# Optimization experiments

Hardware: AMD Instinct MI355X
Metric: run time of the kernel (lower is better)

The kernel has to match this reference:

```python
import jax, jax.numpy as jnp
import numpy as np

B, T, D, H, DK, DV, C, M = 8, 512, 1024, 8, 128, 128, 512, 512
TAU = float(DK) ** 0.5

def _ln(x, g, b, eps=1e-6):
    mu = x.mean(-1, keepdims=True)
    var = ((x - mu) ** 2).mean(-1, keepdims=True)
    return (x - mu) * jax.lax.rsqrt(var + eps) * g + b

def _hln(x, eps=1e-6):
    mu = x.mean(-1, keepdims=True)
    var = ((x - mu) ** 2).mean(-1, keepdims=True)
    return (x - mu) * jax.lax.rsqrt(var + eps)

def setup_inputs() -> dict:
    key = jax.random.key(0)
    ks = jax.random.split(key, 14)
    s = lambda k, shape, fan: jax.random.normal(k, shape, jnp.float32) * (fan ** -0.5)
    return {
        "x": jax.random.normal(ks[0], (B, T, D), jnp.float32),
        "doc_ids": jax.random.randint(ks[1], (B, T), 0, 4),
        "loss_mask": jnp.ones((B, T), jnp.float32),
        "xl_k_hat": jax.random.normal(ks[2], (B, H, M, DK), jnp.float32),
        "xl_v": jax.random.normal(ks[3], (B, H, M, DV), jnp.float32),
        "agg_upper": jax.random.normal(ks[4], (B, H, C, DV), jnp.float32),
        "agg_lower": jax.random.uniform(ks[5], (B, H, C), jnp.float32) * 8.0,
        "w_ln_g": jnp.ones((D,), jnp.float32),
        "w_ln_b": jnp.zeros((D,), jnp.float32),
        "w_q": s(ks[6], (D, H * DK), D),
        "w_k": s(ks[7], (D, H * DK), D),
        "w_v": s(ks[8], (D, H * DV), D),
        "w_g": s(ks[9], (D, H * DV), D),
        "w_res": s(ks[10], (H * DV, D), H * DV),
        "x_u": jax.random.normal(ks[11], (H, DK), jnp.float32) * 0.02,
        "codebook": jax.random.normal(ks[12], (H, C, DK), jnp.float32),
    }

def reference(x, doc_ids, loss_mask, xl_k_hat, xl_v, agg_upper, agg_lower,
              w_ln_g, w_ln_b, w_q, w_k, w_v, w_g, w_res, x_u, codebook):
    # ---- compute_k_q_v_g ----
    xt = _ln(x, w_ln_g, w_ln_b)                                  # [B,T,D]
    q = _hln((xt @ w_q).reshape(B, T, H, DK).transpose(0, 2, 1, 3))  # [B,H,T,DK]
    k = _hln((xt @ w_k).reshape(B, T, H, DK).transpose(0, 2, 1, 3))  # [B,H,T,DK]
    v = (xt @ w_v).reshape(B, T, H, DV).transpose(0, 2, 1, 3)        # [B,H,T,DV]
    g = jax.nn.silu(xt @ w_g)                                        # [B,T,H*DV]

    # ---- vector quantize keys (LearnableVQ) ----
    # dist[b,h,t,c] = ||k - codebook||^2 ; argmin -> shortcodes z
    kc = jnp.einsum('bhtd,hcd->bhtc', k, codebook)
    dist = (k ** 2).sum(-1)[..., None] - 2.0 * kc + (codebook ** 2).sum(-1)[None, :, None, :]
    z = jnp.argmin(dist, axis=-1)                                 # [B,H,T] shortcodes
    k_hat = codebook[jnp.arange(H)[None, :, None], z]             # [B,H,T,DK]
    k_hat_st = k + jax.lax.stop_gradient(k_hat - k)               # straight-through
    mask = loss_mask[:, None, :]                                  # [B,1,T]
    denom_m = mask.sum() * H + 1e-6
    l_commit = (((k - jax.lax.stop_gradient(k_hat)) ** 2).sum(-1) * mask).sum() / denom_m
    l_codebook = (((jax.lax.stop_gradient(k) - k_hat) ** 2).sum(-1) * mask).sum() / denom_m

    # ---- attention over xlcache ++ present, plus aggregated codeword cache ----
    recent_k = jnp.concatenate([xl_k_hat, k_hat_st], axis=2)      # [B,H,M+T,DK]
    recent_v = jnp.concatenate([xl_v, v], axis=2)                 # [B,H,M+T,DV]
    qb = q + x_u[None, :, None, :]
    s_rec = jnp.einsum('bhtd,bhsd->bhts', qb, recent_k) / TAU     # [B,H,T,M+T]
    s_agg = jnp.einsum('bhtd,hcd->bhtc', qb, codebook) / TAU      # [B,H,T,C]

    i = jnp.arange(T)[:, None]
    j = jnp.arange(M + T)[None, :]
    allow = ((j - M) <= i).astype(s_rec.dtype)                    # causal over recent window
    NEG = jnp.asarray(-1e30, s_rec.dtype)
    s_rec_m = jnp.where(allow > 0, s_rec, NEG)

    m = jnp.maximum(s_rec_m.max(-1), s_agg.max(-1))               # [B,H,T]
    a_rec = jnp.exp(s_rec_m - m[..., None]) * allow               # [B,H,T,M+T]
    a_agg = jnp.exp(s_agg - m[..., None])                         # [B,H,T,C]
    den = a_rec.sum(-1) + jnp.einsum('bhtc,bhc->bht', a_agg, agg_lower)
    num = (jnp.einsum('bhts,bhsd->bhtd', a_rec, recent_v)
           + jnp.einsum('bhtc,bhcd->bhtd', a_agg, agg_upper))
    wv = num / den[..., None]                                     # [B,H,T,DV]

    o = wv.transpose(0, 2, 1, 3).reshape(B, T, H * DV) * g        # gated
    res = o @ w_res                                               # [B,T,D]
    return res, l_commit, l_codebook
```

## Files before the change

### kernel.cpp

```cpp
#include <hip/hip_runtime.h>
#include <math.h>

namespace {

constexpr int nB = 8, nT = 512, nD = 1024, nH = 8, nDK = 128, nDV = 128, nC = 512, nM = 512;
constexpr int NROW = nB * nT;
constexpr float RTAU = 0.08838834764831845f;

typedef __attribute__((ext_vector_type(8))) short short8;
typedef __attribute__((ext_vector_type(4))) float f32x4;

__device__ __forceinline__ ushort f2bf(float f) {
  union { float f; uint u; } x; x.f = f;
  uint r = x.u + 0x7fff + ((x.u >> 16) & 1);
  return (ushort)(r >> 16);
}
__device__ __forceinline__ uint pk2(float a, float b) {
  return (uint)f2bf(a) | ((uint)f2bf(b) << 16);
}
__device__ __forceinline__ float bf2f(ushort u) {
  return __uint_as_float(((uint)u) << 16);
}
__device__ __forceinline__ void gload16(const void* g, void* l) {
  __builtin_amdgcn_global_load_lds((const __attribute__((address_space(1))) void*)g,
                                   (__attribute__((address_space(3))) void*)l, 16, 0, 0);
}

constexpr int PREP_LN = 4096;
constexpr int PREP_CAST = PREP_LN + 12288;
constexpr int PREP_WT = PREP_CAST + 1280;
constexpr int PREP_CB = PREP_WT + 2048;

__global__ __launch_bounds__(256) void prep_kernel(
    const float* __restrict__ x, const float* __restrict__ gw, const float* __restrict__ bw,
    ushort* __restrict__ xt_bf,
    const float* __restrict__ xlk, ushort* __restrict__ xlk_bf,
    const float* __restrict__ xlv, ushort* __restrict__ xlv_bf,
    const float* __restrict__ aggU, ushort* __restrict__ aggU_bf,
    const float* __restrict__ wq, const float* __restrict__ wk, const float* __restrict__ wv,
    const float* __restrict__ wg, const float* __restrict__ wres,
    ushort* __restrict__ wqkvg_t, ushort* __restrict__ wres_t,
    const float* __restrict__ cb, float* __restrict__ cbn, ushort* __restrict__ cb_bf) {
  __shared__ float tile[64][65];
  __shared__ float smc[4];
  const int bid = blockIdx.x;
  const int tid = threadIdx.x;

  if (bid < PREP_LN) {
    size_t row = bid;
    float4 v = ((const float4*)(x + row * nD))[tid];
    {
      int lane = tid & 63, w = tid >> 6;
      float s = v.x + v.y + v.z + v.w;
#pragma unroll
      for (int off = 32; off; off >>= 1) s += __shfl_down(s, off);
      if (lane == 0) smc[w] = s;
    }
    __syncthreads();
    float mu = (smc[0] + smc[1] + smc[2] + smc[3]) * (1.f / nD);
    __syncthreads();
    float4 d = make_float4(v.x - mu, v.y - mu, v.z - mu, v.w - mu);
    {
      int lane = tid & 63, w = tid >> 6;
      float s = d.x * d.x + d.y * d.y + d.z * d.z + d.w * d.w;
#pragma unroll
      for (int off = 32; off; off >>= 1) s += __shfl_down(s, off);
      if (lane == 0) smc[w] = s;
    }
    __syncthreads();
    float var = (smc[0] + smc[1] + smc[2] + smc[3]) * (1.f / nD);
    float rs = rsqrtf(var + 1e-6f);
    float4 gg = ((const float4*)gw)[tid];
    float4 bb = ((const float4*)bw)[tid];
    uint2 pb;
    pb.x = pk2(d.x * rs * gg.x + bb.x, d.y * rs * gg.y + bb.y);
    pb.y = pk2(d.z * rs * gg.z + bb.z, d.w * rs * gg.w + bb.w);
    ((uint2*)(xt_bf + row * nD))[tid] = pb;
  } else if (bid < PREP_CAST) {
    const int i = bid - PREP_LN;
    const int which = i >> 12, blk = i & 4095;
    const float* src = which == 0 ? xlk : (which == 1 ? xlv : aggU);
    ushort* dst = which == 0 ? xlk_bf : (which == 1 ? xlv_bf : aggU_bf);
    size_t idx = (size_t)blk * 256 + tid;
    float4 v = ((const float4*)src)[idx];
    uint2 p;
    p.x = pk2(v.x, v.y);
    p.y = pk2(v.z, v.w);
    ((uint2*)dst)[idx] = p;
  } else if (bid < PREP_WT) {
    const int i = bid - PREP_CAST;
    const int z = i >> 8, rem = i & 255;
    const int kz = (rem >> 4) * 64, nz = (rem & 15) * 64;
    const float* W;
    ushort* D;
    if (z == 0)      { W = wq;   D = wqkvg_t; }
    else if (z == 1) { W = wk;   D = wqkvg_t + (size_t)1024 * 1024; }
    else if (z == 2) { W = wv;   D = wqkvg_t + (size_t)2048 * 1024; }
    else if (z == 3) { W = wg;   D = wqkvg_t + (size_t)3072 * 1024; }
    else             { W = wres; D = wres_t; }
    const int c = tid & 63, r4 = tid >> 6;
#pragma unroll
    for (int k = 0; k < 16; ++k) {
      int r = k * 4 + r4;
      tile[r][c] = W[(size_t)(kz + r) * 1024 + nz + c];
    }
    __syncthreads();
#pragma unroll
    for (int k = 0; k < 16; ++k) {
      int n = k * 4 + r4;
      D[(size_t)(nz + n) * 1024 + kz + c] = f2bf(tile[c][n]);
    }
  } else {
    const int i = bid - PREP_WT;
    const int grp = tid >> 7, t128 = tid & 127;
    const int hc = i * 2 + grp;
    float v = cb[(size_t)hc * 128 + t128];
    cb_bf[(size_t)hc * 128 + t128] = f2bf(v);
    float s = v * v;
#pragma unroll
    for (int off = 32; off; off >>= 1) s += __shfl_down(s, off);
    if ((t128 & 63) == 0) smc[grp * 2 + (t128 >> 6)] = s;
    __syncthreads();
    if (t128 == 0) cbn[hc] = smc[grp * 2] + smc[grp * 2 + 1];
  }
}

template <int MODE>
__global__ __launch_bounds__(256) void gemm_bf16_kernel(const ushort* __restrict__ A,
                                                        const ushort* __restrict__ Bt,
                                                        float* __restrict__ C0,
                                                        ushort* __restrict__ C1,
                                                        ushort* __restrict__ C2,
                                                        ushort* __restrict__ C3) {
  __shared__ __align__(16) ushort As[128 * 32];
  __shared__ __align__(16) ushort Bs[128 * 32];
  const int tid = threadIdx.x;
  const int w = tid >> 6, l = tid & 63;
  const int lr = l & 15, lg = l >> 4;
  const int wr = w >> 1, wc = w & 1;
  const int n0 = blockIdx.x * 128;
  const int m0 = blockIdx.y * 128;
  constexpr int K = 1024;

  f32x4 acc[4][4];
#pragma unroll
  for (int i = 0; i < 4; ++i)
#pragma unroll
    for (int j = 0; j < 4; ++j) acc[i][j] = (f32x4){0.f, 0.f, 0.f, 0.f};

  const int e0 = w * 512 + l * 8;
  const int r0 = e0 >> 5, c0 = e0 & 31;
  const int e1 = 2048 + e0;
  const int r1 = e1 >> 5, c1 = e1 & 31;
  const ushort* a0p = A + (size_t)(m0 + r0) * K + c0;
  const ushort* a1p = A + (size_t)(m0 + r1) * K + c1;
  const ushort* b0p = Bt + (size_t)(n0 + r0) * K + c0;
  const ushort* b1p = Bt + (size_t)(n0 + r1) * K + c1;
  ushort* lA0 = &As[w * 512];
  ushort* lA1 = &As[2048 + w * 512];
  ushort* lB0 = &Bs[w * 512];
  ushort* lB1 = &Bs[2048 + w * 512];

  for (int k0 = 0; k0 < K; k0 += 32) {
    __syncthreads();
    gload16(a0p + k0, lA0);
    gload16(a1p + k0, lA1);
    gload16(b0p + k0, lB0);
    gload16(b1p + k0, lB1);
    __syncthreads();
    short8 af[4], bfr[4];
#pragma unroll
    for (int i = 0; i < 4; ++i) af[i] = *(const short8*)&As[(wr * 64 + i * 16 + lr) * 32 + lg * 8];
#pragma unroll
    for (int j = 0; j < 4; ++j) bfr[j] = *(const short8*)&Bs[(wc * 64 + j * 16 + lr) * 32 + lg * 8];
    __builtin_amdgcn_s_setprio(1);
#pragma unroll
    for (int i = 0; i < 4; ++i)
#pragma unroll
      for (int j = 0; j < 4; ++j)
        acc[i][j] = __builtin_amdgcn_mfma_f32_16x16x32_bf16(af[i], bfr[j], acc[i][j], 0, 0, 0);
    __builtin_amdgcn_s_setprio(0);
  }

  const int seg = n0 >> 10;
  const int nbase = n0 & 1023;
#pragma unroll
  for (int i = 0; i < 4; ++i)
#pragma unroll
    for (int j = 0; j < 4; ++j)
#pragma unroll
      for (int r2 = 0; r2 < 4; ++r2) {
        const int row = m0 + wr * 64 + i * 16 + lg * 4 + r2;
        const int col = wc * 64 + j * 16 + lr;
        float v = acc[i][j][r2];
        if (MODE == 0) {
          C0[(size_t)row * 1024 + n0 + col] = v;
        } else {
          const int nloc = nbase + col;
          if (seg == 0)      C1[(size_t)row * 1024 + nloc] = f2bf(v);
          else if (seg == 1) C0[(size_t)row * 1024 + nloc] = v;
          else if (seg == 2) C2[(size_t)row * 1024 + nloc] = f2bf(v);
          else {
            float s = v / (1.f + __expf(-v));
            C3[(size_t)row * 1024 + nloc] = f2bf(s);
          }
        }
      }
}

__global__ __launch_bounds__(256) void hln_both_kernel(ushort* __restrict__ qbuf,
                                                       const float* __restrict__ xu,
                                                       float* __restrict__ kbuf,
                                                       ushort* __restrict__ kbf,
                                                       float* __restrict__ knorm2) {
  int lane = threadIdx.x & 63;
  size_t row = (size_t)blockIdx.x * 4 + (threadIdx.x >> 6);
  if (blockIdx.y == 0) {
    ushort* p = qbuf + row * 128;
    uint u = *(uint*)(p + lane * 2);
    float vx = bf2f((ushort)(u & 0xffff)), vy = bf2f((ushort)(u >> 16));
    float s = vx + vy;
#pragma unroll
    for (int off = 32; off; off >>= 1) s += __shfl_down(s, off);
    float mu = __shfl(s, 0) * (1.f / 128.f);
    float dx = vx - mu, dy = vy - mu;
    float q = dx * dx + dy * dy;
#pragma unroll
    for (int off = 32; off; off >>= 1) q += __shfl_down(q, off);
    float rs = rsqrtf(__shfl(q, 0) * (1.f / 128.f) + 1e-6f);
    int h = (int)(row & 7);
    float ox = dx * rs + xu[h * 128 + lane * 2];
    float oy = dy * rs + xu[h * 128 + lane * 2 + 1];
    *(uint*)(p + lane * 2) = pk2(ox, oy);
  } else {
    float* p = kbuf + row * 128;
    float2 v = *(float2*)(p + lane * 2);
    float s = v.x + v.y;
#pragma unroll
    for (int off = 32; off; off >>= 1) s += __shfl_down(s, off);
    float mu = __shfl(s, 0) * (1.f / 128.f);
    float dx = v.x - mu, dy = v.y - mu;
    float q = dx * dx + dy * dy;
#pragma unroll
    for (int off = 32; off; off >>= 1) q += __shfl_down(q, off);
    float qf = __shfl(q, 0);
    float rs = rsqrtf(qf * (1.f / 128.f) + 1e-6f);
    float ox = dx * rs, oy = dy * rs;
    *(uint*)(kbf + row * 128 + lane * 2) = pk2(ox, oy);
    if (lane == 0) knorm2[row] = qf * rs * rs;
  }
}

__global__ __launch_bounds__(256) void vq_mfma_kernel(const ushort* __restrict__ kbf,
                                                      const ushort* __restrict__ cb_bf,
                                                      const float* __restrict__ cbn,
                                                      const float* __restrict__ knorm2,
                                                      const float* __restrict__ mask,
                                                      ushort* __restrict__ khat_bf,
                                                      float* __restrict__ blocksq) {
  __shared__ ushort Kb[64][136];
  __shared__ ushort Cb[64][136];
  __shared__ float cnsh[64];
  __shared__ int zsh[64];
  __shared__ float dsh[64];
  const int tid = threadIdx.x;
  const int w = tid >> 6, l = tid & 63;
  const int lr = l & 15, lg = l >> 4;
  const int b = blockIdx.y >> 3, h = blockIdx.y & 7;
  const int t0 = blockIdx.x * 64;
  const int srow = tid >> 2, sd = (tid & 3) * 32;

  {
    const ushort* src = kbf + ((size_t)((b * nT + t0 + srow) * nH + h)) * 128 + sd;
    *(uint4*)&Kb[srow][sd] = *(const uint4*)src;
    *(uint4*)&Kb[srow][sd + 8] = *(const uint4*)(src + 8);
    *(uint4*)&Kb[srow][sd + 16] = *(const uint4*)(src + 16);
    *(uint4*)&Kb[srow][sd + 24] = *(const uint4*)(src + 24);
  }
  __syncthreads();

  short8 af[4];
#pragma unroll
  for (int k0 = 0; k0 < 4; ++k0) af[k0] = *(const short8*)&Kb[w * 16 + lr][k0 * 32 + lg * 8];

  float best[4] = {1e30f, 1e30f, 1e30f, 1e30f};
  int bidx[4] = {0, 0, 0, 0};

  for (int cc = 0; cc < 8; ++cc) {
    __syncthreads();
    {
      const ushort* src = cb_bf + ((size_t)(h * nC + cc * 64 + srow)) * 128 + sd;
      *(uint4*)&Cb[srow][sd] = *(const uint4*)src;
      *(uint4*)&Cb[srow][sd + 8] = *(const uint4*)(src + 8);
      *(uint4*)&Cb[srow][sd + 16] = *(const uint4*)(src + 16);
      *(uint4*)&Cb[srow][sd + 24] = *(const uint4*)(src + 24);
      if (tid < 64) cnsh[tid] = cbn[h * nC + cc * 64 + tid];
    }
    __syncthreads();
#pragma unroll
    for (int ct = 0; ct < 4; ++ct) {
      f32x4 z = (f32x4){0.f, 0.f, 0.f, 0.f};
#pragma unroll
      for (int k0 = 0; k0 < 4; ++k0) {
        short8 cf = *(const short8*)&Cb[ct * 16 + lr][k0 * 32 + lg * 8];
        z = __builtin_amdgcn_mfma_f32_16x16x32_bf16(af[k0], cf, z, 0, 0, 0);
      }
      const int code = cc * 64 + ct * 16 + lr;
      const float cn = cnsh[ct * 16 + lr];
#pragma unroll
      for (int r2 = 0; r2 < 4; ++r2) {
        float d = cn - 2.f * z[r2];
        if (d < best[r2]) { best[r2] = d; bidx[r2] = code; }
      }
    }
  }

#pragma unroll
  for (int off = 1; off < 16; off <<= 1) {
#pragma unroll
    for (int r2 = 0; r2 < 4; ++r2) {
      float od = __shfl_xor(best[r2], off);
      int oi = __shfl_xor(bidx[r2], off);
      if (od < best[r2] || (od == best[r2] && oi < bidx[r2])) { best[r2] = od; bidx[r2] = oi; }
    }
  }
  if (lr == 0) {
#pragma unroll
    for (int r2 = 0; r2 < 4; ++r2) {
      int row = w * 16 + lg * 4 + r2;
      zsh[row] = bidx[r2];
      dsh[row] = best[r2];
    }
  }
  __syncthreads();

  {
    const int row = tid >> 2, part = (tid & 3) * 32;
    const ushort* src = cb_bf + ((size_t)(h * nC + zsh[row])) * 128 + part;
    ushort* dst = khat_bf + ((size_t)((b * nT + t0 + row) * nH + h)) * 128 + part;
    *(uint4*)dst = *(const uint4*)src;
    *(uint4*)(dst + 8) = *(const uint4*)(src + 8);
    *(uint4*)(dst + 16) = *(const uint4*)(src + 16);
    *(uint4*)(dst + 24) = *(const uint4*)(src + 24);
  }

  if (tid < 64) {
    float s = mask[b * nT + t0 + tid] *
              (knorm2[(size_t)(b * nT + t0 + tid) * nH + h] + dsh[tid]);
#pragma unroll
    for (int off = 32; off; off >>= 1) s += __shfl_down(s, off);
    if (tid == 0) blocksq[blockIdx.y * gridDim.x + blockIdx.x] = s;
  }
}

__global__ __launch_bounds__(256) void attn_mfma_kernel(
    const ushort* __restrict__ qb, const ushort* __restrict__ khat,
    const ushort* __restrict__ vbuf, const ushort* __restrict__ xlk,
    const ushort* __restrict__ xlv, const ushort* __restrict__ cbb,
    const ushort* __restrict__ aggU, const float* __restrict__ aggL,
    const ushort* __restrict__ gbuf, ushort* __restrict__ o) {
  __shared__ ushort Ks[64][136];
  __shared__ ushort Vts[128][72];
  __shared__ ushort Ps[4][16][72];
  __shared__ float lowb[64];

  const int tid = threadIdx.x;
  const int w = tid >> 6, l = tid & 63;
  const int lr = l & 15, lg = l >> 4;
  const int b = blockIdx.x >> 3, h = blockIdx.x & 7;
  const int t0 = blockIdx.y * 64;

  short8 qf[4];
  {
    const ushort* qrow = qb + ((size_t)((b * nT + t0 + w * 16 + lr) * nH + h)) * 128;
#pragma unroll
    for (int k0 = 0; k0 < 4; ++k0) qf[k0] = *(const short8*)(qrow + k0 * 32 + lg * 8);
  }

  float m_r[4] = {-1e30f, -1e30f, -1e30f, -1e30f};
  float l_r[4] = {0.f, 0.f, 0.f, 0.f};
  f32x4 acc_o[8];
#pragma unroll
  for (int dt = 0; dt < 8; ++dt) acc_o[dt] = (f32x4){0.f, 0.f, 0.f, 0.f};

  const int srow = tid >> 2, sd = (tid & 3) * 32;
  const int kp = tid & 31, dbase = (tid >> 5) * 16;

  auto stageK = [&](const ushort* src) {
#pragma unroll
    for (int q4 = 0; q4 < 4; ++q4)
      *(uint4*)&Ks[srow][sd + q4 * 8] = *(const uint4*)(src + q4 * 8);
  };
  auto stageVbf = [&](const ushort* v0, const ushort* v1) {
    short8 a0 = *(const short8*)(v0);
    short8 a1 = *(const short8*)(v0 + 8);
    short8 b0 = *(const short8*)(v1);
    short8 b1 = *(const short8*)(v1 + 8);
#pragma unroll
    for (int i2 = 0; i2 < 8; ++i2) {
      *(uint*)&Vts[dbase + i2][2 * kp] = (uint)(ushort)a0[i2] | ((uint)(ushort)b0[i2] << 16);
      *(uint*)&Vts[dbase + 8 + i2][2 * kp] = (uint)(ushort)a1[i2] | ((uint)(ushort)b1[i2] << 16);
    }
  };

  auto chunk_body = [&](int sbase, bool AGG, bool MASKQ) {
    f32x4 sc[4];
    __builtin_amdgcn_s_setprio(1);
#pragma unroll
    for (int kt = 0; kt < 4; ++kt) {
      f32x4 z = (f32x4){0.f, 0.f, 0.f, 0.f};
#pragma unroll
      for (int k0 = 0; k0 < 4; ++k0) {
        short8 kf = *(const short8*)&Ks[kt * 16 + lr][k0 * 32 + lg * 8];
        z = __builtin_amdgcn_mfma_f32_16x16x32_bf16(qf[k0], kf, z, 0, 0, 0);
      }
      sc[kt] = z;
    }
    __builtin_amdgcn_s_setprio(0);
    float sv[4][4];
    float pm[4] = {-1e30f, -1e30f, -1e30f, -1e30f};
#pragma unroll
    for (int kt = 0; kt < 4; ++kt)
#pragma unroll
      for (int r2 = 0; r2 < 4; ++r2) {
        float s = sc[kt][r2] * RTAU;
        if (MASKQ) {
          int key = sbase + kt * 16 + lr;
          int tl = t0 + w * 16 + lg * 4 + r2 + nM;
          if (key > tl) s = -1e30f;
        }
        sv[kt][r2] = s;
        pm[r2] = fmaxf(pm[r2], s);
      }
#pragma unroll
    for (int r2 = 0; r2 < 4; ++r2)
#pragma unroll
      for (int off = 1; off < 16; off <<= 1) pm[r2] = fmaxf(pm[r2], __shfl_xor(pm[r2], off));
    float scale[4], rs[4];
#pragma unroll
    for (int r2 = 0; r2 < 4; ++r2) {
      float mn = fmaxf(m_r[r2], pm[r2]);
      scale[r2] = __expf(m_r[r2] - mn);
      m_r[r2] = mn;
      rs[r2] = 0.f;
    }
#pragma unroll
    for (int kt = 0; kt < 4; ++kt)
#pragma unroll
      for (int r2 = 0; r2 < 4; ++r2) {
        float p = __expf(sv[kt][r2] - m_r[r2]);
        rs[r2] += AGG ? p * lowb[kt * 16 + lr] : p;
        Ps[w][lg * 4 + r2][kt * 16 + lr] = f2bf(p);
      }
#pragma unroll
    for (int r2 = 0; r2 < 4; ++r2)
#pragma unroll
      for (int off = 1; off < 16; off <<= 1) rs[r2] += __shfl_xor(rs[r2], off);
#pragma unroll
    for (int r2 = 0; r2 < 4; ++r2) l_r[r2] = l_r[r2] * scale[r2] + rs[r2];
#pragma unroll
    for (int dt = 0; dt < 8; ++dt)
#pragma unroll
      for (int r2 = 0; r2 < 4; ++r2) acc_o[dt][r2] *= scale[r2];
    short8 pa0 = *(const short8*)&Ps[w][lr][lg * 8];
    short8 pa1 = *(const short8*)&Ps[w][lr][32 + lg * 8];
    __builtin_amdgcn_s_setprio(1);
#pragma unroll
    for (int dt = 0; dt < 8; ++dt) {
      short8 vf0 = *(const short8*)&Vts[dt * 16 + lr][lg * 8];
      short8 vf1 = *(const short8*)&Vts[dt * 16 + lr][32 + lg * 8];
      acc_o[dt] = __builtin_amdgcn_mfma_f32_16x16x32_bf16(pa0, vf0, acc_o[dt], 0, 0, 0);
      acc_o[dt] = __builtin_amdgcn_mfma_f32_16x16x32_bf16(pa1, vf1, acc_o[dt], 0, 0, 0);
    }
    __builtin_amdgcn_s_setprio(0);
  };

  const int nch = t0 / 64 + 9;
  for (int ci = 0; ci < nch; ++ci) {
    const int sbase = ci * 64;
    __syncthreads();
    {
      int s = sbase + srow;
      const ushort* src = (s < nM)
          ? xlk + ((size_t)(b * nH + h) * nM + s) * 128 + sd
          : khat + ((size_t)((b * nT + (s - nM)) * nH + h)) * 128 + sd;
      stageK(src);
    }
    {
      int s0 = sbase + 2 * kp;
      if (s0 < nM) {
        const ushort* v0 = xlv + ((size_t)(b * nH + h) * nM + s0) * 128 + dbase;
        stageVbf(v0, v0 + 128);
      } else {
        const ushort* v0 = vbuf + ((size_t)((b * nT + (s0 - nM)) * nH + h)) * 128 + dbase;
        stageVbf(v0, v0 + nH * 128);
      }
    }
    __syncthreads();
    chunk_body(sbase, false, ci == nch - 1);
  }

  for (int ca = 0; ca < 8; ++ca) {
    const int sbase = ca * 64;
    __syncthreads();
    stageK(cbb + ((size_t)h * nC + sbase + srow) * 128 + sd);
    {
      const ushort* v0 = aggU + ((size_t)(b * nH + h) * nC + sbase + 2 * kp) * 128 + dbase;
      stageVbf(v0, v0 + 128);
    }
    if (tid < 64) lowb[tid] = aggL[(size_t)(b * nH + h) * nC + sbase + tid];
    __syncthreads();
    chunk_body(sbase, true, false);
  }

  float inv[4];
#pragma unroll
  for (int r2 = 0; r2 < 4; ++r2) inv[r2] = 1.f / l_r[r2];
#pragma unroll
  for (int dt = 0; dt < 8; ++dt)
#pragma unroll
    for (int r2 = 0; r2 < 4; ++r2) {
      int trow = t0 + w * 16 + lg * 4 + r2;
      size_t oi = ((size_t)(b * nT + trow)) * nD + h * 128 + dt * 16 + lr;
      float gv = bf2f(gbuf[oi]);
      o[oi] = f2bf(acc_o[dt][r2] * inv[r2] * gv);
    }
}

__global__ __launch_bounds__(256) void finalize_kernel(const float* __restrict__ blocksq,
                                                       int nblk,
                                                       const float* __restrict__ mask,
                                                       float* __restrict__ outp) {
  __shared__ float sm[8];
  const int tid = threadIdx.x;
  float s = 0.f, ms = 0.f;
  for (int i = tid; i < NROW; i += 256) {
    if (i < nblk) s += blocksq[i];
    ms += mask[i];
  }
#pragma unroll
  for (int off = 32; off; off >>= 1) { s += __shfl_down(s, off); ms += __shfl_down(ms, off); }
  if ((tid & 63) == 0) { sm[tid >> 6] = s; sm[4 + (tid >> 6)] = ms; }
  __syncthreads();
  if (tid == 0) {
    float ts = sm[0] + sm[1] + sm[2] + sm[3];
    float tm = sm[4] + sm[5] + sm[6] + sm[7];
    float l = ts / (tm * (float)nH + 1e-6f);
    outp[0] = l;
    outp[1] = l;
  }
}

}

extern "C" void kernel_launch(void* const* d_in, const int* in_sizes, int n_in,
                              void* d_out, int out_size, void* d_ws, size_t ws_size,
                              hipStream_t stream) {
  const float* x    = (const float*)d_in[0];
  const float* mask = (const float*)d_in[2];
  const float* xlk  = (const float*)d_in[3];
  const float* xlv  = (const float*)d_in[4];
  const float* aggU = (const float*)d_in[5];
  const float* aggL = (const float*)d_in[6];
  const float* wlng = (const float*)d_in[7];
  const float* wlnb = (const float*)d_in[8];
  const float* wq   = (const float*)d_in[9];
  const float* wk   = (const float*)d_in[10];
  const float* wv   = (const float*)d_in[11];
  const float* wg   = (const float*)d_in[12];
  const float* wres = (const float*)d_in[13];
  const float* xu   = (const float*)d_in[14];
  const float* cb   = (const float*)d_in[15];
  float* out = (float*)d_out;

  float* ws = (float*)d_ws;
  const size_t SZ = (size_t)NROW * nD;
  float*  kbuf    = ws;
  ushort* qbuf_bf = (ushort*)(ws + SZ);
  ushort* khat_bf = (ushort*)(ws + SZ + SZ / 2);
  ushort* vbuf_bf = (ushort*)(ws + 2 * SZ);
  ushort* gbuf_bf = (ushort*)(ws + 2 * SZ + SZ / 2);
  ushort* xt_bf   = (ushort*)(ws + 3 * SZ);
  ushort* wqkvg_t = (ushort*)(ws + 3 * SZ + SZ / 2);
  ushort* wres_t  = (ushort*)(ws + 4 * SZ);
  ushort* xlk_bf  = (ushort*)(ws + 4 * SZ + SZ / 8);
  ushort* xlv_bf  = (ushort*)(ws + 4 * SZ + SZ / 8 + SZ / 2);
  ushort* aggU_bf = (ushort*)(ws + 4 * SZ + SZ / 8 + SZ);
  ushort* cb_bf   = (ushort*)(ws + 4 * SZ + SZ / 8 + 3 * SZ / 2);
  float*  cbn     = ws + 4 * SZ + SZ / 8 + 3 * SZ / 2 + SZ / 16;
  float*  knorm2  = cbn + 4096;
  float*  bsq     = knorm2 + 32768;
  ushort* kbf     = xt_bf;
  ushort* obuf_bf = xt_bf;

  prep_kernel<<<PREP_CB, 256, 0, stream>>>(
      x, wlng, wlnb, xt_bf, xlk, xlk_bf, xlv, xlv_bf, aggU, aggU_bf,
      wq, wk, wv, wg, wres, wqkvg_t, wres_t, cb, cbn, cb_bf);

  gemm_bf16_kernel<1><<<dim3(32, 32), 256, 0, stream>>>(xt_bf, wqkvg_t, kbuf,
                                                        qbuf_bf, vbuf_bf, gbuf_bf);

  hln_both_kernel<<<dim3((NROW * nH) / 4, 2), 256, 0, stream>>>(qbuf_bf, xu,
                                                                kbuf, kbf, knorm2);

  vq_mfma_kernel<<<dim3(nT / 64, nB * nH), 256, 0, stream>>>(kbf, cb_bf, cbn, knorm2,
                                                             mask, khat_bf, bsq);

  attn_mfma_kernel<<<dim3(nB * nH, nT / 64), 256, 0, stream>>>(
      qbuf_bf, khat_bf, vbuf_bf, xlk_bf, xlv_bf, cb_bf, aggU_bf, aggL, gbuf_bf, obuf_bf);

  gemm_bf16_kernel<0><<<dim3(8, 32), 256, 0, stream>>>(obuf_bf, wres_t, out,
                                                       nullptr, nullptr, nullptr);
  finalize_kernel<<<1, 256, 0, stream>>>(bsq, nT / 64 * nB * nH, mask, out + SZ);
}
```

Before: 239.5 us.

## Split attention into recent and codebook partitions with a separate combine kernel

The attention kernel now launches twice as many blocks. Each query tile runs either the recent-window (XL memory plus causal) chunks or the codebook-aggregate chunks. Each block writes its unnormalized numerator in bf16 plus its running max and denominator. A new combine kernel merges the two partials with log-sum-exp rescaling and applies the normalization and gate. The aim is more parallelism and shorter per-block serial chunk loops on a grid that previously had only 512 blocks. In exchange it adds partial-result traffic through global memory, an extra launch, and bf16 rounding of the unnormalized numerators.

```diff
diff --git a/kernel.cpp b/kernel.cpp
--- a/kernel.cpp
+++ b/kernel.cpp
@@ -5,6 +5,7 @@
 
 constexpr int nB = 8, nT = 512, nD = 1024, nH = 8, nDK = 128, nDV = 128, nC = 512, nM = 512;
 constexpr int NROW = nB * nT;
+constexpr int NROWH = NROW * nH;
 constexpr float RTAU = 0.08838834764831845f;
 
 typedef __attribute__((ext_vector_type(8))) short short8;
@@ -353,12 +354,12 @@
   }
 }
 
-__global__ __launch_bounds__(256) void attn_mfma_kernel(
+__global__ __launch_bounds__(256) void attn_split_kernel(
     const ushort* __restrict__ qb, const ushort* __restrict__ khat,
     const ushort* __restrict__ vbuf, const ushort* __restrict__ xlk,
     const ushort* __restrict__ xlv, const ushort* __restrict__ cbb,
     const ushort* __restrict__ aggU, const float* __restrict__ aggL,
-    const ushort* __restrict__ gbuf, ushort* __restrict__ o) {
+    ushort* __restrict__ pnum, float* __restrict__ pml) {
   __shared__ ushort Ks[64][136];
   __shared__ ushort Vts[128][72];
   __shared__ ushort Ps[4][16][72];
@@ -368,7 +369,8 @@
   const int w = tid >> 6, l = tid & 63;
   const int lr = l & 15, lg = l >> 4;
   const int b = blockIdx.x >> 3, h = blockIdx.x & 7;
-  const int t0 = blockIdx.y * 64;
+  const int t0 = (blockIdx.y >> 1) * 64;
+  const int part = blockIdx.y & 1;
 
   short8 qf[4];
   {
@@ -475,56 +477,87 @@
     __builtin_amdgcn_s_setprio(0);
   };
 
-  const int nch = t0 / 64 + 9;
-  for (int ci = 0; ci < nch; ++ci) {
-    const int sbase = ci * 64;
-    __syncthreads();
-    {
-      int s = sbase + srow;
-      const ushort* src = (s < nM)
-          ? xlk + ((size_t)(b * nH + h) * nM + s) * 128 + sd
-          : khat + ((size_t)((b * nT + (s - nM)) * nH + h)) * 128 + sd;
-      stageK(src);
-    }
-    {
-      int s0 = sbase + 2 * kp;
-      if (s0 < nM) {
-        const ushort* v0 = xlv + ((size_t)(b * nH + h) * nM + s0) * 128 + dbase;
+  if (part == 0) {
+    const int nch = t0 / 64 + 9;
+    for (int ci = 0; ci < nch; ++ci) {
+      const int sbase = ci * 64;
+      __syncthreads();
+      {
+        int s = sbase + srow;
+        const ushort* src = (s < nM)
+            ? xlk + ((size_t)(b * nH + h) * nM + s) * 128 + sd
+            : khat + ((size_t)((b * nT + (s - nM)) * nH + h)) * 128 + sd;
+        stageK(src);
+      }
+      {
+        int s0 = sbase + 2 * kp;
+        if (s0 < nM) {
+          const ushort* v0 = xlv + ((size_t)(b * nH + h) * nM + s0) * 128 + dbase;
+          stageVbf(v0, v0 + 128);
+        } else {
+          const ushort* v0 = vbuf + ((size_t)((b * nT + (s0 - nM)) * nH + h)) * 128 + dbase;
+          stageVbf(v0, v0 + nH * 128);
+        }
+      }
+      __syncthreads();
+      chunk_body(sbase, false, ci == nch - 1);
+    }
+  } else {
+    for (int ca = 0; ca < 8; ++ca) {
+      const int sbase = ca * 64;
+      __syncthreads();
+      stageK(cbb + ((size_t)h * nC + sbase + srow) * 128 + sd);
+      {
+        const ushort* v0 = aggU + ((size_t)(b * nH + h) * nC + sbase + 2 * kp) * 128 + dbase;
         stageVbf(v0, v0 + 128);
-      } else {
-        const ushort* v0 = vbuf + ((size_t)((b * nT + (s0 - nM)) * nH + h)) * 128 + dbase;
-        stageVbf(v0, v0 + nH * 128);
-      }
-    }
-    __syncthreads();
-    chunk_body(sbase, false, ci == nch - 1);
-  }
-
-  for (int ca = 0; ca < 8; ++ca) {
-    const int sbase = ca * 64;
-    __syncthreads();
-    stageK(cbb + ((size_t)h * nC + sbase + srow) * 128 + sd);
-    {
-      const ushort* v0 = aggU + ((size_t)(b * nH + h) * nC + sbase + 2 * kp) * 128 + dbase;
-      stageVbf(v0, v0 + 128);
-    }
-    if (tid < 64) lowb[tid] = aggL[(size_t)(b * nH + h) * nC + sbase + tid];
-    __syncthreads();
-    chunk_body(sbase, true, false);
-  }
-
-  float inv[4];
-#pragma unroll
-  for (int r2 = 0; r2 < 4; ++r2) inv[r2] = 1.f / l_r[r2];
+      }
+      if (tid < 64) lowb[tid] = aggL[(size_t)(b * nH + h) * nC + sbase + tid];
+      __syncthreads();
+      chunk_body(sbase, true, false);
+    }
+  }
+
+  ushort* pn = pnum + (size_t)part * NROWH * 128;
+  float* pmlp = pml + (size_t)part * NROWH * 2;
 #pragma unroll
   for (int dt = 0; dt < 8; ++dt)
 #pragma unroll
     for (int r2 = 0; r2 < 4; ++r2) {
       int trow = t0 + w * 16 + lg * 4 + r2;
-      size_t oi = ((size_t)(b * nT + trow)) * nD + h * 128 + dt * 16 + lr;
-      float gv = bf2f(gbuf[oi]);
-      o[oi] = f2bf(acc_o[dt][r2] * inv[r2] * gv);
-    }
+      size_t idx = (size_t)(b * nT + trow) * nH + h;
+      pn[idx * 128 + dt * 16 + lr] = f2bf(acc_o[dt][r2]);
+    }
+  if (lr == 0) {
+#pragma unroll
+    for (int r2 = 0; r2 < 4; ++r2) {
+      int trow = t0 + w * 16 + lg * 4 + r2;
+      size_t idx = (size_t)(b * nT + trow) * nH + h;
+      pmlp[idx * 2] = m_r[r2];
+      pmlp[idx * 2 + 1] = l_r[r2];
+    }
+  }
+}
+
+__global__ __launch_bounds__(256) void combine_kernel(const ushort* __restrict__ pnum,
+                                                      const float* __restrict__ pml,
+                                                      const ushort* __restrict__ gbuf,
+                                                      ushort* __restrict__ o) {
+  int lane = threadIdx.x & 63;
+  size_t idx = (size_t)blockIdx.x * 4 + (threadIdx.x >> 6);
+  float m0 = pml[idx * 2], l0 = pml[idx * 2 + 1];
+  float m1 = pml[(size_t)NROWH * 2 + idx * 2], l1 = pml[(size_t)NROWH * 2 + idx * 2 + 1];
+  float m = fmaxf(m0, m1);
+  float c0 = __expf(m0 - m), c1 = __expf(m1 - m);
+  float inv = 1.f / (l0 * c0 + l1 * c1);
+  uint u0 = *(const uint*)(pnum + idx * 128 + lane * 2);
+  uint u1 = *(const uint*)(pnum + (size_t)NROWH * 128 + idx * 128 + lane * 2);
+  size_t oi = (idx >> 3) * nD + (idx & 7) * 128 + lane * 2;
+  uint gu = *(const uint*)(gbuf + oi);
+  float nx = bf2f((ushort)(u0 & 0xffff)) * c0 + bf2f((ushort)(u1 & 0xffff)) * c1;
+  float ny = bf2f((ushort)(u0 >> 16)) * c0 + bf2f((ushort)(u1 >> 16)) * c1;
+  float ox = nx * inv * bf2f((ushort)(gu & 0xffff));
+  float oy = ny * inv * bf2f((ushort)(gu >> 16));
+  *(uint*)(o + oi) = pk2(ox, oy);
 }
 
 __global__ __launch_bounds__(256) void finalize_kernel(const float* __restrict__ blocksq,
@@ -590,8 +623,10 @@
   float*  cbn     = ws + 4 * SZ + SZ / 8 + 3 * SZ / 2 + SZ / 16;
   float*  knorm2  = cbn + 4096;
   float*  bsq     = knorm2 + 32768;
+  float*  pml     = bsq + 512;
   ushort* kbf     = xt_bf;
   ushort* obuf_bf = xt_bf;
+  ushort* pnum    = (ushort*)kbuf;
 
   prep_kernel<<<PREP_CB, 256, 0, stream>>>(
       x, wlng, wlnb, xt_bf, xlk, xlk_bf, xlv, xlv_bf, aggU, aggU_bf,
@@ -606,8 +641,10 @@
   vq_mfma_kernel<<<dim3(nT / 64, nB * nH), 256, 0, stream>>>(kbf, cb_bf, cbn, knorm2,
                                                              mask, khat_bf, bsq);
 
-  attn_mfma_kernel<<<dim3(nB * nH, nT / 64), 256, 0, stream>>>(
-      qbuf_bf, khat_bf, vbuf_bf, xlk_bf, xlv_bf, cb_bf, aggU_bf, aggL, gbuf_bf, obuf_bf);
+  attn_split_kernel<<<dim3(nB * nH, (nT / 64) * 2), 256, 0, stream>>>(
+      qbuf_bf, khat_bf, vbuf_bf, xlk_bf, xlv_bf, cb_bf, aggU_bf, aggL, pnum, pml);
+
+  combine_kernel<<<NROWH / 4, 256, 0, stream>>>(pnum, pml, gbuf_bf, obuf_bf);
 
   gemm_bf16_kernel<0><<<dim3(8, 32), 256, 0, stream>>>(obuf_bf, wres_t, out,
                                                        nullptr, nullptr, nullptr);
```

Result: slower. 252.8 us (+5.5%).

## Fuse headwise LayerNorm of q and k into the QKVG GEMM epilogue

Applied to the files above, without the earlier changes.

Computes per-head row mean and variance directly from GEMM accumulators using shuffle reductions and a small shared-memory exchange between the two column-waves, then writes normalized bf16 q (with x_u bias) and k plus key norms. This removes the separate hln kernel and the fp32 k round trip through global memory. Variance now uses a one-pass sum-of-squares formula, which is slightly less numerically robust, and the epilogue adds a block barrier.

```diff
diff --git a/kernel.cpp b/kernel.cpp
--- a/kernel.cpp
+++ b/kernel.cpp
@@ -131,9 +131,14 @@
                                                         float* __restrict__ C0,
                                                         ushort* __restrict__ C1,
                                                         ushort* __restrict__ C2,
-                                                        ushort* __restrict__ C3) {
+                                                        ushort* __restrict__ C3,
+                                                        ushort* __restrict__ kbf,
+                                                        float* __restrict__ knorm2,
+                                                        const float* __restrict__ xu) {
   __shared__ __align__(16) ushort As[128 * 32];
   __shared__ __align__(16) ushort Bs[128 * 32];
+  __shared__ float rowsum[128][2];
+  __shared__ float rowsum2[128][2];
   const int tid = threadIdx.x;
   const int w = tid >> 6, l = tid & 63;
   const int lr = l & 15, lg = l >> 4;
@@ -184,70 +189,85 @@
 
   const int seg = n0 >> 10;
   const int nbase = n0 & 1023;
-#pragma unroll
-  for (int i = 0; i < 4; ++i)
-#pragma unroll
-    for (int j = 0; j < 4; ++j)
+  if (MODE == 1 && seg <= 1) {
+    const int h = nbase >> 7;
+    float ps[4][4], ps2[4][4];
+#pragma unroll
+    for (int i = 0; i < 4; ++i)
 #pragma unroll
       for (int r2 = 0; r2 < 4; ++r2) {
-        const int row = m0 + wr * 64 + i * 16 + lg * 4 + r2;
-        const int col = wc * 64 + j * 16 + lr;
-        float v = acc[i][j][r2];
-        if (MODE == 0) {
-          C0[(size_t)row * 1024 + n0 + col] = v;
-        } else {
-          const int nloc = nbase + col;
-          if (seg == 0)      C1[(size_t)row * 1024 + nloc] = f2bf(v);
-          else if (seg == 1) C0[(size_t)row * 1024 + nloc] = v;
-          else if (seg == 2) C2[(size_t)row * 1024 + nloc] = f2bf(v);
-          else {
-            float s = v / (1.f + __expf(-v));
-            C3[(size_t)row * 1024 + nloc] = f2bf(s);
+        float s = 0.f, s2 = 0.f;
+#pragma unroll
+        for (int j = 0; j < 4; ++j) {
+          float v = acc[i][j][r2];
+          s += v;
+          s2 += v * v;
+        }
+#pragma unroll
+        for (int off = 1; off < 16; off <<= 1) {
+          s += __shfl_xor(s, off);
+          s2 += __shfl_xor(s2, off);
+        }
+        ps[i][r2] = s;
+        ps2[i][r2] = s2;
+      }
+    if (lr == 0) {
+#pragma unroll
+      for (int i = 0; i < 4; ++i)
+#pragma unroll
+        for (int r2 = 0; r2 < 4; ++r2) {
+          int rloc = wr * 64 + i * 16 + lg * 4 + r2;
+          rowsum[rloc][wc] = ps[i][r2];
+          rowsum2[rloc][wc] = ps2[i][r2];
+        }
+    }
+    __syncthreads();
+#pragma unroll
+    for (int i = 0; i < 4; ++i)
+#pragma unroll
+      for (int r2 = 0; r2 < 4; ++r2) {
+        const int rloc = wr * 64 + i * 16 + lg * 4 + r2;
+        const int grow = m0 + rloc;
+        float tot = rowsum[rloc][0] + rowsum[rloc][1];
+        float tot2 = rowsum2[rloc][0] + rowsum2[rloc][1];
+        float mu = tot * (1.f / 128.f);
+        float qf = tot2 - 128.f * mu * mu;
+        float rs = rsqrtf(qf * (1.f / 128.f) + 1e-6f);
+#pragma unroll
+        for (int j = 0; j < 4; ++j) {
+          const int col = wc * 64 + j * 16 + lr;
+          float v = (acc[i][j][r2] - mu) * rs;
+          if (seg == 0) {
+            v += xu[h * 128 + col];
+            C1[(size_t)grow * 1024 + nbase + col] = f2bf(v);
+          } else {
+            kbf[(size_t)grow * 1024 + nbase + col] = f2bf(v);
           }
         }
-      }
-}
-
-__global__ __launch_bounds__(256) void hln_both_kernel(ushort* __restrict__ qbuf,
-                                                       const float* __restrict__ xu,
-                                                       float* __restrict__ kbuf,
-                                                       ushort* __restrict__ kbf,
-                                                       float* __restrict__ knorm2) {
-  int lane = threadIdx.x & 63;
-  size_t row = (size_t)blockIdx.x * 4 + (threadIdx.x >> 6);
-  if (blockIdx.y == 0) {
-    ushort* p = qbuf + row * 128;
-    uint u = *(uint*)(p + lane * 2);
-    float vx = bf2f((ushort)(u & 0xffff)), vy = bf2f((ushort)(u >> 16));
-    float s = vx + vy;
-#pragma unroll
-    for (int off = 32; off; off >>= 1) s += __shfl_down(s, off);
-    float mu = __shfl(s, 0) * (1.f / 128.f);
-    float dx = vx - mu, dy = vy - mu;
-    float q = dx * dx + dy * dy;
-#pragma unroll
-    for (int off = 32; off; off >>= 1) q += __shfl_down(q, off);
-    float rs = rsqrtf(__shfl(q, 0) * (1.f / 128.f) + 1e-6f);
-    int h = (int)(row & 7);
-    float ox = dx * rs + xu[h * 128 + lane * 2];
-    float oy = dy * rs + xu[h * 128 + lane * 2 + 1];
-    *(uint*)(p + lane * 2) = pk2(ox, oy);
+        if (seg == 1 && lr == 0 && wc == 0) knorm2[(size_t)grow * 8 + h] = qf * rs * rs;
+      }
   } else {
-    float* p = kbuf + row * 128;
-    float2 v = *(float2*)(p + lane * 2);
-    float s = v.x + v.y;
-#pragma unroll
-    for (int off = 32; off; off >>= 1) s += __shfl_down(s, off);
-    float mu = __shfl(s, 0) * (1.f / 128.f);
-    float dx = v.x - mu, dy = v.y - mu;
-    float q = dx * dx + dy * dy;
-#pragma unroll
-    for (int off = 32; off; off >>= 1) q += __shfl_down(q, off);
-    float qf = __shfl(q, 0);
-    float rs = rsqrtf(qf * (1.f / 128.f) + 1e-6f);
-    float ox = dx * rs, oy = dy * rs;
-    *(uint*)(kbf + row * 128 + lane * 2) = pk2(ox, oy);
-    if (lane == 0) knorm2[row] = qf * rs * rs;
+#pragma unroll
+    for (int i = 0; i < 4; ++i)
+#pragma unroll
+      for (int j = 0; j < 4; ++j)
+#pragma unroll
+        for (int r2 = 0; r2 < 4; ++r2) {
+          const int row = m0 + wr * 64 + i * 16 + lg * 4 + r2;
+          const int col = wc * 64 + j * 16 + lr;
+          float v = acc[i][j][r2];
+          if (MODE == 0) {
+            C0[(size_t)row * 1024 + n0 + col] = v;
+          } else {
+            const int nloc = nbase + col;
+            if (seg == 2) {
+              C2[(size_t)row * 1024 + nloc] = f2bf(v);
+            } else {
+              float s = v / (1.f + __expf(-v));
+              C3[(size_t)row * 1024 + nloc] = f2bf(s);
+            }
+          }
+        }
   }
 }
 
@@ -575,7 +595,7 @@
 
   float* ws = (float*)d_ws;
   const size_t SZ = (size_t)NROW * nD;
-  float*  kbuf    = ws;
+  float*  kregion = ws;
   ushort* qbuf_bf = (ushort*)(ws + SZ);
   ushort* khat_bf = (ushort*)(ws + SZ + SZ / 2);
   ushort* vbuf_bf = (ushort*)(ws + 2 * SZ);
@@ -590,18 +610,15 @@
   float*  cbn     = ws + 4 * SZ + SZ / 8 + 3 * SZ / 2 + SZ / 16;
   float*  knorm2  = cbn + 4096;
   float*  bsq     = knorm2 + 32768;
-  ushort* kbf     = xt_bf;
+  ushort* kbf     = (ushort*)kregion;
   ushort* obuf_bf = xt_bf;
 
   prep_kernel<<<PREP_CB, 256, 0, stream>>>(
       x, wlng, wlnb, xt_bf, xlk, xlk_bf, xlv, xlv_bf, aggU, aggU_bf,
       wq, wk, wv, wg, wres, wqkvg_t, wres_t, cb, cbn, cb_bf);
 
-  gemm_bf16_kernel<1><<<dim3(32, 32), 256, 0, stream>>>(xt_bf, wqkvg_t, kbuf,
-                                                        qbuf_bf, vbuf_bf, gbuf_bf);
-
-  hln_both_kernel<<<dim3((NROW * nH) / 4, 2), 256, 0, stream>>>(qbuf_bf, xu,
-                                                                kbuf, kbf, knorm2);
+  gemm_bf16_kernel<1><<<dim3(32, 32), 256, 0, stream>>>(
+      xt_bf, wqkvg_t, nullptr, qbuf_bf, vbuf_bf, gbuf_bf, kbf, knorm2, xu);
 
   vq_mfma_kernel<<<dim3(nT / 64, nB * nH), 256, 0, stream>>>(kbf, cb_bf, cbn, knorm2,
                                                              mask, khat_bf, bsq);
@@ -609,7 +626,7 @@
   attn_mfma_kernel<<<dim3(nB * nH, nT / 64), 256, 0, stream>>>(
       qbuf_bf, khat_bf, vbuf_bf, xlk_bf, xlv_bf, cb_bf, aggU_bf, aggL, gbuf_bf, obuf_bf);
 
-  gemm_bf16_kernel<0><<<dim3(8, 32), 256, 0, stream>>>(obuf_bf, wres_t, out,
-                                                       nullptr, nullptr, nullptr);
+  gemm_bf16_kernel<0><<<dim3(8, 32), 256, 0, stream>>>(
+      obuf_bf, wres_t, out, nullptr, nullptr, nullptr, nullptr, nullptr, nullptr);
   finalize_kernel<<<1, 256, 0, stream>>>(bsq, nT / 64 * nB * nH, mask, out + SZ);
 }
```

Measured after the change: 231.2 us. 3.5% less time.
